# Optimization experiments

Measured on AMD Instinct MI355X. Metric: run time of the kernel, lower is better.

Reference implementation:

```python
import jax, jax.numpy as jnp
import numpy as np

N_HEAD = 16
DIM = 1024
DIM_HEAD = DIM // N_HEAD
B, S = 4, 2048


def setup_inputs() -> dict:
    key = jax.random.key(0)
    ks = jax.random.split(key, 12)
    p = lambda k, shape: jax.random.normal(k, shape, dtype=jnp.float32) * 0.02
    return {
        "query": jax.random.normal(ks[0], (B, S, DIM), dtype=jnp.float32),
        "key": jax.random.normal(ks[1], (B, S, DIM), dtype=jnp.float32),
        "value": jax.random.normal(ks[2], (B, S, DIM), dtype=jnp.float32),
        "mask": jnp.zeros((B, 1, S, S), dtype=bool),
        "w_q": p(ks[3], (DIM, DIM)), "b_q": jnp.zeros((DIM,), jnp.float32),
        "w_k": p(ks[4], (DIM, DIM)), "b_k": jnp.zeros((DIM,), jnp.float32),
        "w_v": p(ks[5], (DIM, DIM)), "b_v": jnp.zeros((DIM,), jnp.float32),
        "w_o": p(ks[6], (DIM, DIM)), "b_o": jnp.zeros((DIM,), jnp.float32),
    }


def _split_heads(x):
    b, s, _ = x.shape
    return x.reshape(b, s, N_HEAD, DIM_HEAD).transpose(0, 2, 1, 3)  # [b,h,s,dh]


def reference(query, key, value, mask, w_q, b_q, w_k, b_k, w_v, b_v, w_o, b_o):
    # QKV projections (torch Linear: x @ W^T + b)
    Q = _split_heads(query @ w_q.T + b_q)
    K = _split_heads(key @ w_k.T + b_k)
    V = _split_heads(value @ w_v.T + b_v)
    scale = 1.0 / np.sqrt(DIM_HEAD).astype(np.float32)
    scores = jnp.einsum("bhqd,bhkd->bhqk", Q, K) * scale  # [b,h,sq,sk]
    scores = jnp.where(mask, -jnp.inf, scores)
    probs = jax.nn.softmax(scores, axis=-1)
    attn = jnp.einsum("bhqk,bhkd->bhqd", probs, V)
    b, h, s, dh = attn.shape
    merged = attn.transpose(0, 2, 1, 3).reshape(b, s, h * dh)
    return merged @ w_o.T + b_o
```

## Files before the change

### kernel.cpp

```cpp
#include <hip/hip_runtime.h>
#include <hip/hip_bf16.h>
#include <stdint.h>

#define B_N 4
#define S_N 2048
#define DIM_N 1024
#define H_N 16
#define DH_N 64
#define M_ROWS (B_N * S_N)
#define BH_N (B_N * H_N)
#define C1 0.18033688011112042f

typedef unsigned short u16;
typedef __attribute__((ext_vector_type(8))) short short8;
typedef __attribute__((ext_vector_type(4))) float f32x4;
typedef __attribute__((ext_vector_type(16))) float f32x16;

typedef __attribute__((address_space(1))) const void gvoid_t;
typedef __attribute__((address_space(3))) void lvoid_t;

__device__ __forceinline__ u16 f2bf(float f) {
  union { float f; uint32_t u; } c; c.f = f;
  uint32_t u = c.u;
  return (u16)((u + 0x7FFFu + ((u >> 16) & 1u)) >> 16);
}

__device__ __forceinline__ uint32_t pk2(float lo, float hi) {
  float2 f; f.x = lo; f.y = hi;
  __hip_bfloat162 h = __float22bfloat162_rn(f);
  union { __hip_bfloat162 h; uint32_t u; } c; c.h = h;
  return c.u;
}

__global__ void cvt3_kernel(const float* __restrict__ s0, const float* __restrict__ s1,
                            const float* __restrict__ s2, u16* __restrict__ d0,
                            u16* __restrict__ d1, u16* __restrict__ d2_, int n4) {
  const int y = blockIdx.y;
  const float* s = (y == 0) ? s0 : (y == 1 ? s1 : s2);
  u16* d = (y == 0) ? d0 : (y == 1 ? d1 : d2_);
  int i = blockIdx.x * blockDim.x + threadIdx.x;
  if (i >= n4) return;
  float4 v = reinterpret_cast<const float4*>(s)[i];
  ushort4 o;
  o.x = f2bf(v.x); o.y = f2bf(v.y); o.z = f2bf(v.z); o.w = f2bf(v.w);
  reinterpret_cast<ushort4*>(d)[i] = o;
}

__global__ void cvt4_kernel(const float* __restrict__ s0, const float* __restrict__ s1,
                            const float* __restrict__ s2, const float* __restrict__ s3,
                            u16* __restrict__ d0, u16* __restrict__ d1,
                            u16* __restrict__ d2_, u16* __restrict__ d3, int n4) {
  const int y = blockIdx.y;
  const float* s = (y == 0) ? s0 : (y == 1 ? s1 : (y == 2 ? s2 : s3));
  u16* d = (y == 0) ? d0 : (y == 1 ? d1 : (y == 2 ? d2_ : d3));
  int i = blockIdx.x * blockDim.x + threadIdx.x;
  if (i >= n4) return;
  float4 v = reinterpret_cast<const float4*>(s)[i];
  ushort4 o;
  o.x = f2bf(v.x); o.y = f2bf(v.y); o.z = f2bf(v.z); o.w = f2bf(v.w);
  reinterpret_cast<ushort4*>(d)[i] = o;
}

__global__ void pack_mask(const uint8_t* __restrict__ m, uint32_t* __restrict__ bits, int nwords) {
  int i = blockIdx.x * blockDim.x + threadIdx.x;
  if (i >= nwords) return;
  const uint32_t* p = reinterpret_cast<const uint32_t*>(m) + (size_t)i * 8;
  uint32_t out = 0;
#pragma unroll
  for (int w = 0; w < 8; ++w) {
    uint32_t v = p[w];
    if (v & 0x000000FFu) out |= 1u << (w * 4 + 0);
    if (v & 0x0000FF00u) out |= 1u << (w * 4 + 1);
    if (v & 0x00FF0000u) out |= 1u << (w * 4 + 2);
    if (v & 0xFF000000u) out |= 1u << (w * 4 + 3);
  }
  bits[i] = out;
}

__global__ __launch_bounds__(256)
void gemm_qkv(const u16* __restrict__ qb, const u16* __restrict__ kb,
              const u16* __restrict__ vb, const u16* __restrict__ wq,
              const u16* __restrict__ wk, const u16* __restrict__ wv,
              const float* __restrict__ bq, const float* __restrict__ bk,
              const float* __restrict__ bv, u16* __restrict__ Qh,
              u16* __restrict__ Kh, u16* __restrict__ Vt)
{
  __shared__ __align__(16) u16 As[128 * 32];
  __shared__ __align__(16) u16 Bs[128 * 32];
  const int z = blockIdx.z;
  const u16* A  = (z == 0) ? qb : (z == 1 ? kb : vb);
  const u16* Bw = (z == 0) ? wq : (z == 1 ? wk : wv);
  const float* bias = (z == 0) ? bq : (z == 1 ? bk : bv);
  u16* outp = (z == 0) ? Qh : (z == 1 ? Kh : Vt);
  const float scale = (z == 0) ? C1 : 1.0f;

  const int m0 = blockIdx.x * 128, n0 = blockIdx.y * 128;
  const int t = threadIdx.x, w = t >> 6;
  const int l = t & 63, lr = l & 15, lg = l >> 4;
  const int wr = (w >> 1) * 64, wc = (w & 1) * 64;
  const int srow = t >> 2;
  const int skoff = (t & 3) * 8;

  f32x4 acc[4][4] = {};

  for (int k0 = 0; k0 < DIM_N; k0 += 32) {
    __syncthreads();
#pragma unroll
    for (int c = 0; c < 2; ++c) {
      const u16* ga = A  + (size_t)(m0 + c * 64 + srow) * DIM_N + k0 + skoff;
      const u16* gb = Bw + (size_t)(n0 + c * 64 + srow) * DIM_N + k0 + skoff;
      u16* la = &As[(c * 64 + 16 * w) * 32];
      u16* lb = &Bs[(c * 64 + 16 * w) * 32];
      __builtin_amdgcn_global_load_lds((gvoid_t*)ga, (lvoid_t*)la, 16, 0, 0);
      __builtin_amdgcn_global_load_lds((gvoid_t*)gb, (lvoid_t*)lb, 16, 0, 0);
    }
    __syncthreads();

    short8 af[4], bfr[4];
#pragma unroll
    for (int mf = 0; mf < 4; ++mf)
      af[mf] = *reinterpret_cast<const short8*>(&As[(wr + mf * 16 + lr) * 32 + lg * 8]);
#pragma unroll
    for (int nf = 0; nf < 4; ++nf)
      bfr[nf] = *reinterpret_cast<const short8*>(&Bs[(wc + nf * 16 + lr) * 32 + lg * 8]);
#pragma unroll
    for (int mf = 0; mf < 4; ++mf)
#pragma unroll
      for (int nf = 0; nf < 4; ++nf)
        acc[mf][nf] = __builtin_amdgcn_mfma_f32_16x16x32_bf16(af[mf], bfr[nf], acc[mf][nf], 0, 0, 0);
  }

  float bv4[4];
#pragma unroll
  for (int nf = 0; nf < 4; ++nf) bv4[nf] = bias[n0 + wc + nf * 16 + lr];

#pragma unroll
  for (int mf = 0; mf < 4; ++mf)
#pragma unroll
    for (int nf = 0; nf < 4; ++nf)
#pragma unroll
      for (int r = 0; r < 4; ++r) {
        int grow = m0 + wr + mf * 16 + lg * 4 + r;
        int gcol = n0 + wc + nf * 16 + lr;
        float v = (acc[mf][nf][r] + bv4[nf]) * scale;
        int b = grow >> 11, s = grow & 2047;
        int h = gcol >> 6, d = gcol & 63;
        size_t idx;
        if (z < 2) {
          idx = ((size_t)(b * H_N + h) * S_N + s) * DH_N + d;
        } else {
          int sp = ((((s & 15) + 4) & 8) ? (s ^ 12) : s);
          idx = ((size_t)(b * H_N + h) * DH_N + d) * S_N + sp;
        }
        outp[idx] = f2bf(v);
      }
}

__global__ __launch_bounds__(256)
void gemm_out(const u16* __restrict__ A, const u16* __restrict__ Bw,
              const float* __restrict__ bias, float* __restrict__ outp)
{
  __shared__ __align__(16) u16 As[128 * 32];
  __shared__ __align__(16) u16 Bs[128 * 32];
  const int m0 = blockIdx.x * 128, n0 = blockIdx.y * 128;
  const int t = threadIdx.x, w = t >> 6;
  const int l = t & 63, lr = l & 15, lg = l >> 4;
  const int wr = (w >> 1) * 64, wc = (w & 1) * 64;
  const int srow = t >> 2;
  const int skoff = (t & 3) * 8;

  f32x4 acc[4][4] = {};

  for (int k0 = 0; k0 < DIM_N; k0 += 32) {
    __syncthreads();
#pragma unroll
    for (int c = 0; c < 2; ++c) {
      const u16* ga = A  + (size_t)(m0 + c * 64 + srow) * DIM_N + k0 + skoff;
      const u16* gb = Bw + (size_t)(n0 + c * 64 + srow) * DIM_N + k0 + skoff;
      u16* la = &As[(c * 64 + 16 * w) * 32];
      u16* lb = &Bs[(c * 64 + 16 * w) * 32];
      __builtin_amdgcn_global_load_lds((gvoid_t*)ga, (lvoid_t*)la, 16, 0, 0);
      __builtin_amdgcn_global_load_lds((gvoid_t*)gb, (lvoid_t*)lb, 16, 0, 0);
    }
    __syncthreads();

    short8 af[4], bfr[4];
#pragma unroll
    for (int mf = 0; mf < 4; ++mf)
      af[mf] = *reinterpret_cast<const short8*>(&As[(wr + mf * 16 + lr) * 32 + lg * 8]);
#pragma unroll
    for (int nf = 0; nf < 4; ++nf)
      bfr[nf] = *reinterpret_cast<const short8*>(&Bs[(wc + nf * 16 + lr) * 32 + lg * 8]);
#pragma unroll
    for (int mf = 0; mf < 4; ++mf)
#pragma unroll
      for (int nf = 0; nf < 4; ++nf)
        acc[mf][nf] = __builtin_amdgcn_mfma_f32_16x16x32_bf16(af[mf], bfr[nf], acc[mf][nf], 0, 0, 0);
  }

  float bv4[4];
#pragma unroll
  for (int nf = 0; nf < 4; ++nf) bv4[nf] = bias[n0 + wc + nf * 16 + lr];

#pragma unroll
  for (int mf = 0; mf < 4; ++mf)
#pragma unroll
    for (int nf = 0; nf < 4; ++nf)
#pragma unroll
      for (int r = 0; r < 4; ++r) {
        int grow = m0 + wr + mf * 16 + lg * 4 + r;
        int gcol = n0 + wc + nf * 16 + lr;
        outp[(size_t)grow * DIM_N + gcol] = acc[mf][nf][r] + bv4[nf];
      }
}

#define AT_WAVES 4
#define QPW 64
#define KVB 64
#define NCH (S_N / KVB)

__global__ __launch_bounds__(256, 2)
void attn_kernel(const u16* __restrict__ Qh, const u16* __restrict__ Kh,
                 const u16* __restrict__ Vt, const uint32_t* __restrict__ mbits,
                 u16* __restrict__ AO)
{
  __shared__ __align__(16) u16 K_lds[2][KVB * DH_N];
  __shared__ __align__(16) u16 V_lds[2][DH_N * KVB];

  const int t = threadIdx.x;
  const int w = t >> 6, l = t & 63;
  const int l31 = l & 31, hl = l >> 5;
  const int kx = l31 & 7;

  const int bx = blockIdx.x;
  const int bh = (bx & 7) * 8 + (bx >> 3);
  const int b = bh >> 4, h = bh & 15;
  const int q0 = blockIdx.y * (AT_WAVES * QPW) + w * QPW;

  const u16* Qp = Qh + (size_t)bh * S_N * DH_N;
  const u16* Kp = Kh + (size_t)bh * S_N * DH_N;
  const u16* Vp = Vt + (size_t)bh * DH_N * S_N;
  const uint32_t* mrow0 = mbits + ((size_t)b * S_N + q0 + l31) * (S_N / 32);
  const uint32_t* mrow1 = mbits + ((size_t)b * S_N + q0 + 32 + l31) * (S_N / 32);

  short8 qf0[4], qf1[4];
#pragma unroll
  for (int u = 0; u < 4; ++u) {
    qf0[u] = *reinterpret_cast<const short8*>(
        Qp + (size_t)(q0 + l31) * DH_N + u * 16 + hl * 8);
    qf1[u] = *reinterpret_cast<const short8*>(
        Qp + (size_t)(q0 + 32 + l31) * DH_N + u * 16 + hl * 8);
  }

  f32x16 o00 = {}, o01 = {}, o10 = {}, o11 = {};
  float lr0 = 0.f, lr1 = 0.f;

  auto STAGE = [&](int buf, int kc) {
#pragma unroll
    for (int p = 0; p < 2; ++p) {
      const int s = p * 256 + t;
      const int row = s >> 3, up = s & 7, j = up ^ (row & 7);
      const u16* gk = Kp + (size_t)(kc * KVB + row) * DH_N + j * 8;
      const u16* gv = Vp + (size_t)row * S_N + kc * KVB + j * 8;
      u16* lk = &K_lds[buf][(p * 256 + w * 64) * 8];
      u16* lv = &V_lds[buf][(p * 256 + w * 64) * 8];
      __builtin_amdgcn_global_load_lds((gvoid_t*)gk, (lvoid_t*)lk, 16, 0, 0);
      __builtin_amdgcn_global_load_lds((gvoid_t*)gv, (lvoid_t*)lv, 16, 0, 0);
    }
  };

  auto softpv = [&](f32x16& z, uint32_t mw, float& lr,
                    f32x16& oA, f32x16& oB, const short8 vf[2][2]) {
    if (mw) {
#pragma unroll
      for (int r = 0; r < 16; ++r)
        if ((mw >> ((r & 3) + 8 * (r >> 2) + 4 * hl)) & 1) z[r] = -1e30f;
    }

    float p[16];
#pragma unroll
    for (int r = 0; r < 16; ++r) p[r] = __builtin_amdgcn_exp2f(z[r]);
    float a8[8], a4[4];
#pragma unroll
    for (int r = 0; r < 8; ++r) a8[r] = p[2 * r] + p[2 * r + 1];
#pragma unroll
    for (int r = 0; r < 4; ++r) a4[r] = a8[2 * r] + a8[2 * r + 1];
    lr += (a4[0] + a4[1]) + (a4[2] + a4[3]);

    union { uint32_t u[4]; short8 s8; } pf0, pf1;
    pf0.u[0] = pk2(p[0], p[1]);   pf0.u[1] = pk2(p[2], p[3]);
    pf0.u[2] = pk2(p[4], p[5]);   pf0.u[3] = pk2(p[6], p[7]);
    pf1.u[0] = pk2(p[8], p[9]);   pf1.u[1] = pk2(p[10], p[11]);
    pf1.u[2] = pk2(p[12], p[13]); pf1.u[3] = pk2(p[14], p[15]);

    __builtin_amdgcn_s_setprio(1);
    oA = __builtin_amdgcn_mfma_f32_32x32x16_bf16(vf[0][0], pf0.s8, oA, 0, 0, 0);
    oB = __builtin_amdgcn_mfma_f32_32x32x16_bf16(vf[0][1], pf0.s8, oB, 0, 0, 0);
    oA = __builtin_amdgcn_mfma_f32_32x32x16_bf16(vf[1][0], pf1.s8, oA, 0, 0, 0);
    oB = __builtin_amdgcn_mfma_f32_32x32x16_bf16(vf[1][1], pf1.s8, oB, 0, 0, 0);
    __builtin_amdgcn_s_setprio(0);
  };

  auto half = [&](int buf, int hh, uint32_t mwg0, uint32_t mwg1) {
    const int kb = hh * 32;
    short8 kf[4];
#pragma unroll
    for (int u = 0; u < 4; ++u)
      kf[u] = *reinterpret_cast<const short8*>(
          &K_lds[buf][(kb + l31) * DH_N + (((2 * u + hl) ^ kx) * 8)]);

    f32x16 z0 = {}, z1 = {};
    __builtin_amdgcn_s_setprio(1);
    z0 = __builtin_amdgcn_mfma_f32_32x32x16_bf16(kf[0], qf0[0], z0, 0, 0, 0);
    z1 = __builtin_amdgcn_mfma_f32_32x32x16_bf16(kf[0], qf1[0], z1, 0, 0, 0);
    z0 = __builtin_amdgcn_mfma_f32_32x32x16_bf16(kf[1], qf0[1], z0, 0, 0, 0);
    z1 = __builtin_amdgcn_mfma_f32_32x32x16_bf16(kf[1], qf1[1], z1, 0, 0, 0);
    z0 = __builtin_amdgcn_mfma_f32_32x32x16_bf16(kf[2], qf0[2], z0, 0, 0, 0);
    z1 = __builtin_amdgcn_mfma_f32_32x32x16_bf16(kf[2], qf1[2], z1, 0, 0, 0);
    z0 = __builtin_amdgcn_mfma_f32_32x32x16_bf16(kf[3], qf0[3], z0, 0, 0, 0);
    z1 = __builtin_amdgcn_mfma_f32_32x32x16_bf16(kf[3], qf1[3], z1, 0, 0, 0);
    __builtin_amdgcn_s_setprio(0);

    short8 vf[2][2];
#pragma unroll
    for (int ks = 0; ks < 2; ++ks)
#pragma unroll
      for (int nf = 0; nf < 2; ++nf)
        vf[ks][nf] = *reinterpret_cast<const short8*>(
            &V_lds[buf][(nf * 32 + l31) * KVB + (((hh * 4 + ks * 2 + hl) ^ kx) * 8)]);

    softpv(z0, mwg0, lr0, o00, o01, vf);
    softpv(z1, mwg1, lr1, o10, o11, vf);
  };

  STAGE(0, 0);
  __syncthreads();
  int cb = 0;
  for (int kc = 0; kc < NCH; ++kc) {
    uint32_t mw00 = mrow0[2 * kc],     mw10 = mrow1[2 * kc];
    uint32_t mw01 = mrow0[2 * kc + 1], mw11 = mrow1[2 * kc + 1];
    if (kc + 1 < NCH) STAGE(cb ^ 1, kc + 1);
    half(cb, 0, mw00, mw10);
    half(cb, 1, mw01, mw11);
    __syncthreads();
    cb ^= 1;
  }

  auto fin = [&](float lr, int qg, const f32x16& oA, const f32x16& oB) {
    float l_tot = lr + __shfl_xor(lr, 32);
    float inv_l = 1.0f / l_tot;
    u16* orow = AO + ((size_t)b * S_N + q0 + qg + l31) * DIM_N + h * DH_N;
#pragma unroll
    for (int gg = 0; gg < 4; ++gg) {
      ushort4 v4;
      v4.x = f2bf(oA[gg * 4 + 0] * inv_l);
      v4.y = f2bf(oA[gg * 4 + 1] * inv_l);
      v4.z = f2bf(oA[gg * 4 + 2] * inv_l);
      v4.w = f2bf(oA[gg * 4 + 3] * inv_l);
      *reinterpret_cast<ushort4*>(orow + gg * 8 + hl * 4) = v4;
      ushort4 w4;
      w4.x = f2bf(oB[gg * 4 + 0] * inv_l);
      w4.y = f2bf(oB[gg * 4 + 1] * inv_l);
      w4.z = f2bf(oB[gg * 4 + 2] * inv_l);
      w4.w = f2bf(oB[gg * 4 + 3] * inv_l);
      *reinterpret_cast<ushort4*>(orow + 32 + gg * 8 + hl * 4) = w4;
    }
  };
  fin(lr0, 0, o00, o01);
  fin(lr1, 32, o10, o11);
}

extern "C" void kernel_launch(void* const* d_in, const int* in_sizes, int n_in,
                              void* d_out, int out_size, void* d_ws, size_t ws_size,
                              hipStream_t stream)
{
  const float*   q_in = (const float*)d_in[0];
  const float*   k_in = (const float*)d_in[1];
  const float*   v_in = (const float*)d_in[2];
  const uint8_t* mask = (const uint8_t*)d_in[3];
  const float*   w_q  = (const float*)d_in[4];
  const float*   b_q  = (const float*)d_in[5];
  const float*   w_k  = (const float*)d_in[6];
  const float*   b_k  = (const float*)d_in[7];
  const float*   w_v  = (const float*)d_in[8];
  const float*   b_v  = (const float*)d_in[9];
  const float*   w_o  = (const float*)d_in[10];
  const float*   b_o  = (const float*)d_in[11];

  char* ws = (char*)d_ws;
  size_t off = 0;
  auto alloc = [&](size_t bytes) -> char* {
    char* p = ws + off;
    off += (bytes + 255) & ~(size_t)255;
    return p;
  };
  const size_t act_b = (size_t)M_ROWS * DIM_N * 2;
  const size_t w_b   = (size_t)DIM_N * DIM_N * 2;
  const int    nmw   = B_N * S_N * (S_N / 32);
  u16* qb  = (u16*)alloc(act_b);
  u16* kb  = (u16*)alloc(act_b);
  u16* vb  = (u16*)alloc(act_b);
  u16* wqb = (u16*)alloc(w_b);
  u16* wkb = (u16*)alloc(w_b);
  u16* wvb = (u16*)alloc(w_b);
  u16* wob = (u16*)alloc(w_b);
  u16* Qh  = (u16*)alloc(act_b);
  u16* Kh  = (u16*)alloc(act_b);
  u16* Vt  = (u16*)alloc(act_b);
  uint32_t* mbits = (uint32_t*)alloc((size_t)nmw * 4);
  u16* AO  = qb;

  const int n4a = M_ROWS * DIM_N / 4;
  const int n4w = DIM_N * DIM_N / 4;
  cvt3_kernel<<<dim3(n4a / 256, 3), 256, 0, stream>>>(q_in, k_in, v_in, qb, kb, vb, n4a);
  cvt4_kernel<<<dim3(n4w / 256, 4), 256, 0, stream>>>(w_q, w_k, w_v, w_o,
                                                      wqb, wkb, wvb, wob, n4w);
  pack_mask<<<nmw / 256, 256, 0, stream>>>(mask, mbits, nmw);

  gemm_qkv<<<dim3(M_ROWS / 128, DIM_N / 128, 3), 256, 0, stream>>>(
      qb, kb, vb, wqb, wkb, wvb, b_q, b_k, b_v, Qh, Kh, Vt);

  attn_kernel<<<dim3(64, 8), 256, 0, stream>>>(Qh, Kh, Vt, mbits, AO);

  gemm_out<<<dim3(M_ROWS / 128, DIM_N / 128), 256, 0, stream>>>(
      AO, wob, b_o, (float*)d_out);
}
```

Baseline: 229.4 us.

## Software-pipeline QK^T MFMAs of next half-tile ahead of current softmax

```diff
diff --git a/kernel.cpp b/kernel.cpp
--- a/kernel.cpp
+++ b/kernel.cpp
@@ -269,6 +269,36 @@
     }
   };
 
+  auto ldQK = [&](int buf, int hh, f32x16& z0, f32x16& z1) {
+    const int kb = hh * 32;
+    short8 kf[4];
+#pragma unroll
+    for (int u = 0; u < 4; ++u)
+      kf[u] = *reinterpret_cast<const short8*>(
+          &K_lds[buf][(kb + l31) * DH_N + (((2 * u + hl) ^ kx) * 8)]);
+    f32x16 a = {}, c = {};
+    __builtin_amdgcn_s_setprio(1);
+    a = __builtin_amdgcn_mfma_f32_32x32x16_bf16(kf[0], qf0[0], a, 0, 0, 0);
+    c = __builtin_amdgcn_mfma_f32_32x32x16_bf16(kf[0], qf1[0], c, 0, 0, 0);
+    a = __builtin_amdgcn_mfma_f32_32x32x16_bf16(kf[1], qf0[1], a, 0, 0, 0);
+    c = __builtin_amdgcn_mfma_f32_32x32x16_bf16(kf[1], qf1[1], c, 0, 0, 0);
+    a = __builtin_amdgcn_mfma_f32_32x32x16_bf16(kf[2], qf0[2], a, 0, 0, 0);
+    c = __builtin_amdgcn_mfma_f32_32x32x16_bf16(kf[2], qf1[2], c, 0, 0, 0);
+    a = __builtin_amdgcn_mfma_f32_32x32x16_bf16(kf[3], qf0[3], a, 0, 0, 0);
+    c = __builtin_amdgcn_mfma_f32_32x32x16_bf16(kf[3], qf1[3], c, 0, 0, 0);
+    __builtin_amdgcn_s_setprio(0);
+    z0 = a; z1 = c;
+  };
+
+  auto ldV = [&](int buf, int hh, short8 vf[2][2]) {
+#pragma unroll
+    for (int ks = 0; ks < 2; ++ks)
+#pragma unroll
+      for (int nf = 0; nf < 2; ++nf)
+        vf[ks][nf] = *reinterpret_cast<const short8*>(
+            &V_lds[buf][(nf * 32 + l31) * KVB + (((hh * 4 + ks * 2 + hl) ^ kx) * 8)]);
+  };
+
   auto softpv = [&](f32x16& z, uint32_t mw, float& lr,
                     f32x16& oA, f32x16& oB, const short8 vf[2][2]) {
     if (mw) {
@@ -301,48 +331,28 @@
     __builtin_amdgcn_s_setprio(0);
   };
 
-  auto half = [&](int buf, int hh, uint32_t mwg0, uint32_t mwg1) {
-    const int kb = hh * 32;
-    short8 kf[4];
-#pragma unroll
-    for (int u = 0; u < 4; ++u)
-      kf[u] = *reinterpret_cast<const short8*>(
-          &K_lds[buf][(kb + l31) * DH_N + (((2 * u + hl) ^ kx) * 8)]);
-
-    f32x16 z0 = {}, z1 = {};
-    __builtin_amdgcn_s_setprio(1);
-    z0 = __builtin_amdgcn_mfma_f32_32x32x16_bf16(kf[0], qf0[0], z0, 0, 0, 0);
-    z1 = __builtin_amdgcn_mfma_f32_32x32x16_bf16(kf[0], qf1[0], z1, 0, 0, 0);
-    z0 = __builtin_amdgcn_mfma_f32_32x32x16_bf16(kf[1], qf0[1], z0, 0, 0, 0);
-    z1 = __builtin_amdgcn_mfma_f32_32x32x16_bf16(kf[1], qf1[1], z1, 0, 0, 0);
-    z0 = __builtin_amdgcn_mfma_f32_32x32x16_bf16(kf[2], qf0[2], z0, 0, 0, 0);
-    z1 = __builtin_amdgcn_mfma_f32_32x32x16_bf16(kf[2], qf1[2], z1, 0, 0, 0);
-    z0 = __builtin_amdgcn_mfma_f32_32x32x16_bf16(kf[3], qf0[3], z0, 0, 0, 0);
-    z1 = __builtin_amdgcn_mfma_f32_32x32x16_bf16(kf[3], qf1[3], z1, 0, 0, 0);
-    __builtin_amdgcn_s_setprio(0);
-
-    short8 vf[2][2];
-#pragma unroll
-    for (int ks = 0; ks < 2; ++ks)
-#pragma unroll
-      for (int nf = 0; nf < 2; ++nf)
-        vf[ks][nf] = *reinterpret_cast<const short8*>(
-            &V_lds[buf][(nf * 32 + l31) * KVB + (((hh * 4 + ks * 2 + hl) ^ kx) * 8)]);
-
-    softpv(z0, mwg0, lr0, o00, o01, vf);
-    softpv(z1, mwg1, lr1, o10, o11, vf);
-  };
-
   STAGE(0, 0);
   __syncthreads();
+  f32x16 zA0, zA1, zB0, zB1;
+  short8 vfA[2][2], vfB[2][2];
+  ldQK(0, 0, zA0, zA1);
+  ldV(0, 0, vfA);
   int cb = 0;
   for (int kc = 0; kc < NCH; ++kc) {
     uint32_t mw00 = mrow0[2 * kc],     mw10 = mrow1[2 * kc];
     uint32_t mw01 = mrow0[2 * kc + 1], mw11 = mrow1[2 * kc + 1];
     if (kc + 1 < NCH) STAGE(cb ^ 1, kc + 1);
-    half(cb, 0, mw00, mw10);
-    half(cb, 1, mw01, mw11);
+    ldQK(cb, 1, zB0, zB1);
+    ldV(cb, 1, vfB);
+    softpv(zA0, mw00, lr0, o00, o01, vfA);
+    softpv(zA1, mw10, lr1, o10, o11, vfA);
     __syncthreads();
+    if (kc + 1 < NCH) {
+      ldQK(cb ^ 1, 0, zA0, zA1);
+      ldV(cb ^ 1, 0, vfA);
+    }
+    softpv(zB0, mw01, lr0, o00, o01, vfB);
+    softpv(zB1, mw11, lr1, o10, o11, vfB);
     cb ^= 1;
   }
 
```

Result: slower. 252.1 us (+9.9%).
